# Performance work log

Hardware: AMD Instinct MI355X
Metric: run time of the kernel (lower is better)

The kernel has to match this reference:

```python
import jax, jax.numpy as jnp
import numpy as np

H = W = 96                      # image_size (scaled down from (240,240) for working-set control)
K = 16                          # faces_per_pixel
SIGMA = 1e-4
GAMMA = 1e-4
BLUR = float(np.log(1.0 / 1e-4 - 1.0) * SIGMA)   # blur_radius, compared against squared NDC dist (pytorch3d convention)
ZNEAR, ZFAR = 1.0, 100.0        # softmax_rgb_blend defaults
EPS = 1e-10


def _edge_d2(p, a, b):
    # squared point-to-segment distance; p:[B,P,F,2], a,b:[B,1,F,2]
    ab = b - a
    ap = p - a
    t = jnp.clip((ap * ab).sum(-1) / ((ab * ab).sum(-1) + 1e-12), 0.0, 1.0)
    d = ap - t[..., None] * ab
    return (d * d).sum(-1)


def _render(meshes_positions, meshes_rotations, meshes_scale, cam_pos, cam_rot, vertices, vert_colors, faces_packed):
    B, M, _ = meshes_positions.shape
    V = vertices.shape[1]
    # per-mesh scale -> rotate -> translate (forward of MeshesRenderer)
    scaled = meshes_scale[:, :, None, :] * vertices[None]                           # [B,M,V,3]
    world = jnp.einsum('bmij,bmvj->bmvi', meshes_rotations, scaled) + meshes_positions[:, :, None, :]
    world = world.reshape(B, M * V, 3)
    # pytorch3d camera: X_cam = X_world @ R + T
    cam = jnp.einsum('bvj,bji->bvi', world, cam_rot) + cam_pos[:, None, :]
    z = cam[..., 2]                                                                 # [B,N]
    xy = cam[..., :2] / z[..., None]                                                # perspective, focal=1 (NDC)

    tri = xy[:, faces_packed]                                                       # [B,F,3,2]
    tz = z[:, faces_packed]                                                         # [B,F,3]
    fcol = vert_colors.reshape(M * V, 3)[faces_packed]                              # [F,3,3]

    xs = (jnp.arange(W, dtype=xy.dtype) + 0.5) * 2.0 / W - 1.0
    ys = 1.0 - (jnp.arange(H, dtype=xy.dtype) + 0.5) * 2.0 / H
    gx, gy = jnp.meshgrid(xs, ys)
    pix = jnp.stack([gx.ravel(), gy.ravel()], -1)[None, :, None, :]                 # [1,P,1,2]

    v0 = tri[:, None, :, 0]; v1 = tri[:, None, :, 1]; v2 = tri[:, None, :, 2]       # [B,1,F,2]
    e1 = v1 - v0; e2 = v2 - v0
    d = pix - v0                                                                    # [B,P,F,2]
    den = e1[..., 0] * e2[..., 1] - e1[..., 1] * e2[..., 0] + 1e-12
    b1 = (d[..., 0] * e2[..., 1] - d[..., 1] * e2[..., 0]) / den                    # barycentrics [B,P,F]
    b2 = (e1[..., 0] * d[..., 1] - e1[..., 1] * d[..., 0]) / den
    b0 = 1.0 - b1 - b2
    zpix = b0 * tz[:, None, :, 0] + b1 * tz[:, None, :, 1] + b2 * tz[:, None, :, 2]
    inside = (b0 >= 0) & (b1 >= 0) & (b2 >= 0)
    d2 = jnp.minimum(jnp.minimum(_edge_d2(pix, v0, v1), _edge_d2(pix, v1, v2)), _edge_d2(pix, v2, v0))
    dists = jnp.where(inside, -d2, d2)                                              # signed squared dist
    valid = (zpix > 1e-2) & (dists <= BLUR)

    # faces_per_pixel = K nearest faces by depth (z-buffer)
    _, idx = jax.lax.top_k(jnp.where(valid, -zpix, -jnp.inf), K)                    # [B,P,K]
    take = lambda a: jnp.take_along_axis(a, idx, axis=-1)
    bk = jnp.stack([take(b0), take(b1), take(b2)], -1)                              # [B,P,K,3]
    zk, dk = take(zpix), take(dists)
    mk = take(valid.astype(zpix.dtype))
    # texture gather: barycentric blend of per-vertex colors (TexturesVertex.sample_textures)
    texel = jnp.einsum('bpkv,bpkvc->bpkc', bk, fcol[idx])                           # [B,P,K,3]

    # softmax_rgb_blend
    prob = jax.nn.sigmoid(-dk / SIGMA) * mk
    zinv = (ZFAR - zk) / (ZFAR - ZNEAR) * mk
    zmax = jnp.maximum(zinv.max(-1), EPS)
    wnum = prob * jnp.exp((zinv - zmax[..., None]) / GAMMA)
    delta = jnp.exp((EPS - zmax) / GAMMA)
    denom = wnum.sum(-1) + delta
    bg = jnp.ones(3, zpix.dtype)                                                    # default white background
    rgb = ((wnum[..., None] * texel).sum(-2) + delta[..., None] * bg) / denom[..., None]
    alpha = 1.0 - jnp.prod(1.0 - prob, -1)
    return jnp.concatenate([rgb, alpha[..., None]], -1).reshape(B, H, W, 4)


def setup_inputs() -> dict:
    key = jax.random.key(0)
    ks = jax.random.split(key, 8)
    B, M, V, Fm = 2, 2, 256, 256
    vertices = jax.random.normal(ks[0], (M, V, 3), jnp.float32) * 0.4
    faces = jax.random.randint(ks[1], (M, Fm, 3), 0, V)
    vert_colors = jax.random.uniform(ks[2], (M, V, 3), dtype=jnp.float32)
    meshes_positions = jax.random.normal(ks[3], (B, M, 3), jnp.float32) * 0.2
    # small z-axis rotations (proper rotation matrices)
    ang = jax.random.normal(ks[4], (B, M), jnp.float32) * 0.2
    c, s = jnp.cos(ang), jnp.sin(ang)
    z0 = jnp.zeros_like(c); o = jnp.ones_like(c)
    meshes_rotations = jnp.stack([c, -s, z0, s, c, z0, z0, z0, o], -1).reshape(B, M, 3, 3)
    meshes_scale = 1.0 + 0.1 * jax.random.normal(ks[5], (B, M, 3), jnp.float32)
    cam_rot = jnp.tile(jnp.eye(3, dtype=jnp.float32)[None], (B, 1, 1))
    cam_pos = jnp.tile(jnp.array([0.0, 0.0, 3.0], jnp.float32), (B, 1))
    return {
        'meshes_positions': meshes_positions, 'meshes_rotations': meshes_rotations,
        'meshes_scale': meshes_scale, 'cam_pos': cam_pos, 'cam_rot': cam_rot,
        'vertices': vertices, 'faces': faces, 'vert_colors': vert_colors,
    }


def reference(meshes_positions, meshes_rotations, meshes_scale, cam_pos, cam_rot, vertices, faces, vert_colors):
    M, V = vertices.shape[:2]
    faces_packed = (faces + (jnp.arange(M) * V)[:, None, None]).reshape(-1, 3)      # [F,3]
    return _render(meshes_positions, meshes_rotations, meshes_scale, cam_pos, cam_rot,
                   vertices, vert_colors, faces_packed)
```

## Files before the change

kernel.cpp:

```cpp
#include <hip/hip_runtime.h>

#pragma clang fp contract(off)

#define HH 96
#define WW 96
#define KK 16
#define MM 2
#define NF 512
#define NV 512
#define NPIX (HH*WW)
#define TDIM 12
#define TSZ 8
#define NTILE (TDIM*TDIM)
#define MAXC 8
#define BPT 8

#define SIGMA_F 1e-4f
#define GAMMA_F 1e-4f
#define BLUR_F  9.210240366975851e-4f
#define EPS_F   1e-10f
#define ZFAR_F  100.0f
#define ZNEAR_F 1.0f
#define RM      0.0304f

#define SENT 0xFFFFFFFFFFFFFFFFull

__device__ __forceinline__ float frcp(float x) { return __builtin_amdgcn_rcpf(x); }

__device__ __forceinline__ float edge_d2(float px, float py,
                                         float ax, float ay,
                                         float bx, float by) {
    float abx = bx - ax, aby = by - ay;
    float apx = px - ax, apy = py - ay;
    float t = (apx*abx + apy*aby) * frcp(abx*abx + aby*aby + 1e-12f);
    t = fminf(fmaxf(t, 0.0f), 1.0f);
    float dx = apx - t*abx, dy = apy - t*aby;
    return dx*dx + dy*dy;
}

struct Rast { float b0, b1, b2, zpix, dists; };

__device__ __forceinline__ Rast rasterize_s(float px, float py,
                                            float v0x, float v0y, float v1x, float v1y,
                                            float v2x, float v2y,
                                            float z0, float z1, float z2) {
    Rast r;
    float e1x=v1x-v0x, e1y=v1y-v0y, e2x=v2x-v0x, e2y=v2y-v0y;
    float dx=px-v0x, dy=py-v0y;
    float rden = frcp(e1x*e2y - e1y*e2x + 1e-12f);
    r.b1 = (dx*e2y - dy*e2x) * rden;
    r.b2 = (e1x*dy - e1y*dx) * rden;
    r.b0 = 1.0f - r.b1 - r.b2;
    r.zpix = r.b0*z0 + r.b1*z1 + r.b2*z2;
    bool inside = (r.b0 >= 0.0f) && (r.b1 >= 0.0f) && (r.b2 >= 0.0f);
    float d2 = edge_d2(px, py, v0x, v0y, v1x, v1y);
    d2 = fminf(d2, edge_d2(px, py, v1x, v1y, v2x, v2y));
    d2 = fminf(d2, edge_d2(px, py, v2x, v2y, v0x, v0y));
    r.dists = inside ? -d2 : d2;
    return r;
}

__device__ __forceinline__ unsigned long long packzf(float z, int f) {
    return (((unsigned long long)__float_as_uint(z)) << 32) | (unsigned int)f;
}

__device__ __forceinline__ unsigned long long shflx64(unsigned long long v, int m) {
    int lo = __shfl_xor((int)(unsigned)(v & 0xffffffffull), m, 64);
    int hi = __shfl_xor((int)(unsigned)(v >> 32), m, 64);
    return ((unsigned long long)(unsigned)hi << 32) | (unsigned)lo;
}

__global__ __launch_bounds__(512) void render_fused_kernel(
    const float* __restrict__ mpos,
    const float* __restrict__ mrot,
    const float* __restrict__ mscale,
    const float* __restrict__ cpos,
    const float* __restrict__ crot,
    const float* __restrict__ verts,
    const int*   __restrict__ faces,
    const float* __restrict__ vcol,
    float*       __restrict__ out)
{
    const int blocksPerB = NTILE * BPT;
    const int b    = blockIdx.x / blocksPerB;
    const int rem  = blockIdx.x % blocksPerB;
    const int tile = rem / BPT, q = rem % BPT;
    const int wv   = threadIdx.x >> 6;
    const int lane = threadIdx.x & 63;
    const int t    = threadIdx.x;

    __shared__ float svx[NV], svy[NV], svz[NV];
    __shared__ float scr_[NV], scg_[NV], scb_[NV];
    __shared__ float sbx0[NF], sby0[NF], sbx1[NF], sby1[NF];
    __shared__ int   si0[NF], si1[NF], si2[NF];
    __shared__ unsigned short slist[NF];

    float cr[9];
    #pragma unroll
    for (int i = 0; i < 9; ++i) cr[i] = crot[b*9 + i];
    const float cpx = cpos[b*3+0], cpy = cpos[b*3+1], cpz = cpos[b*3+2];

    {
        int g = t;
        int m = g >> 8;
        int sb = (b*MM + m)*3, rb = (b*MM + m)*9;
        float v0 = verts[g*3+0] * mscale[sb+0];
        float v1 = verts[g*3+1] * mscale[sb+1];
        float v2 = verts[g*3+2] * mscale[sb+2];
        float wx = mrot[rb+0]*v0 + mrot[rb+1]*v1 + mrot[rb+2]*v2 + mpos[sb+0];
        float wy = mrot[rb+3]*v0 + mrot[rb+4]*v1 + mrot[rb+5]*v2 + mpos[sb+1];
        float wz = mrot[rb+6]*v0 + mrot[rb+7]*v1 + mrot[rb+8]*v2 + mpos[sb+2];
        float cx = wx*cr[0] + wy*cr[3] + wz*cr[6] + cpx;
        float cy = wx*cr[1] + wy*cr[4] + wz*cr[7] + cpy;
        float cz = wx*cr[2] + wy*cr[5] + wz*cr[8] + cpz;
        svx[g] = cx / cz;  svy[g] = cy / cz;  svz[g] = cz;
        scr_[g] = vcol[g*3+0];
        scg_[g] = vcol[g*3+1];
        scb_[g] = vcol[g*3+2];
    }
    __syncthreads();

    {
        int f = t;
        int off = (f >> 8) << 8;
        int i0 = faces[f*3+0] + off;
        int i1 = faces[f*3+1] + off;
        int i2 = faces[f*3+2] + off;
        si0[f] = i0; si1[f] = i1; si2[f] = i2;
        float x0 = svx[i0], y0 = svy[i0];
        float x1 = svx[i1], y1 = svy[i1];
        float x2 = svx[i2], y2 = svy[i2];
        sbx0[f] = fminf(fminf(x0,x1),x2);
        sby0[f] = fminf(fminf(y0,y1),y2);
        sbx1[f] = fmaxf(fmaxf(x0,x1),x2);
        sby1[f] = fmaxf(fmaxf(y0,y1),y2);
    }
    __syncthreads();

    const int ty = tile / TDIM, tx = tile % TDIM;
    const float x_lo = -1.0f + tx * (2.0f / TDIM);
    const float x_hi = x_lo + 2.0f / TDIM;
    const float y_hi = 1.0f - ty * (2.0f / TDIM);
    const float y_lo = y_hi - 2.0f / TDIM;

    int L = 0;
    #pragma unroll
    for (int k = 0; k < 8; ++k) {
        int f = (k << 6) | lane;
        bool hit = (sbx0[f] - RM <= x_hi) && (sbx1[f] + RM >= x_lo) &&
                   (sby0[f] - RM <= y_hi) && (sby1[f] + RM >= y_lo);
        unsigned long long m = __ballot(hit);
        if (hit) {
            int rank = __popcll(m & ((1ull << lane) - 1ull));
            slist[L + rank] = (unsigned short)f;
        }
        L += __popcll(m);
    }

    const int pi = ty * TSZ + q, pj = tx * TSZ + wv;
    const float px = ((float)pj + 0.5f) * (2.0f / WW) - 1.0f;
    const float py = 1.0f - ((float)pi + 0.5f) * (2.0f / HH);

    unsigned long long pk[MAXC];
    int validm = 0;
    #pragma unroll
    for (int c = 0; c < MAXC; ++c) {
        pk[c] = SENT;
        if (c * 64 < L) {
            int idx = c * 64 + lane;
            int fc = (idx < L) ? (int)slist[idx] : -1;
            unsigned long long tt = SENT;
            if (fc >= 0) {
                int i0 = si0[fc], i1 = si1[fc], i2 = si2[fc];
                Rast r = rasterize_s(px, py, svx[i0], svy[i0], svx[i1], svy[i1],
                                     svx[i2], svy[i2], svz[i0], svz[i1], svz[i2]);
                if (r.zpix > 0.01f && r.dists <= BLUR_F) tt = packzf(r.zpix, fc);
            }
            pk[c] = tt;
            validm |= (tt != SENT ? 1 : 0) << c;
        }
    }

    const int c0 = __popc(validm);
    int cnt = c0;
    #pragma unroll
    for (int m = 1; m < 64; m <<= 1) cnt += __shfl_xor(cnt, m, 64);

    float nr = 0.0f, ng = 0.0f, nb = 0.0f, dn = 0.0f, ap = 1.0f;
    float zmaxv = EPS_F;

#define AGG(ff, zz) do { \
        int f_ = (ff); float z_ = (zz); \
        int i0_ = si0[f_], i1_ = si1[f_], i2_ = si2[f_]; \
        Rast r_ = rasterize_s(px, py, svx[i0_], svy[i0_], svx[i1_], svy[i1_], \
                              svx[i2_], svy[i2_], svz[i0_], svz[i1_], svz[i2_]); \
        float prob_ = frcp(1.0f + __expf(r_.dists / SIGMA_F)); \
        float zinv_ = (ZFAR_F - z_) / (ZFAR_F - ZNEAR_F); \
        float w_ = prob_ * __expf((zinv_ - zmaxv) / GAMMA_F); \
        nr += w_ * (r_.b0*scr_[i0_] + r_.b1*scr_[i1_] + r_.b2*scr_[i2_]); \
        ng += w_ * (r_.b0*scg_[i0_] + r_.b1*scg_[i1_] + r_.b2*scg_[i2_]); \
        nb += w_ * (r_.b0*scb_[i0_] + r_.b1*scb_[i1_] + r_.b2*scb_[i2_]); \
        dn += w_; \
        ap *= (1.0f - prob_); \
    } while (0)

    if (cnt <= KK) {
        unsigned long long lmin = pk[0];
        #pragma unroll
        for (int c = 1; c < MAXC; ++c) lmin = (pk[c] < lmin) ? pk[c] : lmin;
        #pragma unroll
        for (int m = 1; m < 64; m <<= 1) {
            unsigned long long o2 = shflx64(lmin, m);
            lmin = (o2 < lmin) ? o2 : lmin;
        }
        if (cnt > 0) {
            float zming = __uint_as_float((unsigned)(lmin >> 32));
            zmaxv = fmaxf((ZFAR_F - zming) / (ZFAR_F - ZNEAR_F), EPS_F);
        }
        #pragma unroll
        for (int c = 0; c < MAXC; ++c)
            if (validm & (1 << c)) {
                int f = (int)(pk[c] & 0xffffffffull);
                float z = __uint_as_float((unsigned)(pk[c] >> 32));
                AGG(f, z);
            }
    } else if (L <= 64) {
        unsigned long long v = pk[0];
        #pragma unroll
        for (int kk = 2; kk <= 64; kk <<= 1) {
            #pragma unroll
            for (int jj = kk >> 1; jj > 0; jj >>= 1) {
                unsigned long long o2 = shflx64(v, jj);
                bool kmin = ((lane & kk) == 0) == ((lane & jj) == 0);
                v = (kmin == (o2 < v)) ? o2 : v;
            }
        }
        unsigned z0b = (unsigned)__shfl((int)(unsigned)(v >> 32), 0, 64);
        zmaxv = fmaxf((ZFAR_F - __uint_as_float(z0b)) / (ZFAR_F - ZNEAR_F), EPS_F);
        if (lane < KK) {
            int f = (int)(v & 0xffffffffull);
            float z = __uint_as_float((unsigned)(v >> 32));
            AGG(f, z);
        }
    } else {
        int remm = validm, inclm = 0;
        float zming = 0.0f;
        for (int r = 0; r < KK; ++r) {
            unsigned long long lm = SENT;
            #pragma unroll
            for (int k = 0; k < MAXC; ++k)
                if (remm & (1 << k)) lm = (pk[k] < lm) ? pk[k] : lm;
            #pragma unroll
            for (int m = 1; m < 64; m <<= 1) {
                unsigned long long o2 = shflx64(lm, m);
                lm = (o2 < lm) ? o2 : lm;
            }
            if (r == 0) zming = __uint_as_float((unsigned)(lm >> 32));
            #pragma unroll
            for (int k = 0; k < MAXC; ++k)
                if ((remm & (1 << k)) && pk[k] == lm) { inclm |= 1 << k; remm &= ~(1 << k); }
        }
        zmaxv = fmaxf((ZFAR_F - zming) / (ZFAR_F - ZNEAR_F), EPS_F);
        #pragma unroll
        for (int k = 0; k < MAXC; ++k)
            if (inclm & (1 << k)) {
                int f = (int)(pk[k] & 0xffffffffull);
                float z = __uint_as_float((unsigned)(pk[k] >> 32));
                AGG(f, z);
            }
    }
#undef AGG

    #pragma unroll
    for (int m = 1; m < 64; m <<= 1) {
        nr += __shfl_xor(nr, m, 64);
        ng += __shfl_xor(ng, m, 64);
        nb += __shfl_xor(nb, m, 64);
        dn += __shfl_xor(dn, m, 64);
        ap *= __shfl_xor(ap, m, 64);
    }
    if (lane == 0) {
        float delta = __expf((EPS_F - zmaxv) / GAMMA_F);
        float dd = dn + delta;
        float4 o4;
        o4.x = (nr + delta) / dd;
        o4.y = (ng + delta) / dd;
        o4.z = (nb + delta) / dd;
        o4.w = 1.0f - ap;
        *reinterpret_cast<float4*>(&out[((size_t)b * NPIX + pi * WW + pj) * 4]) = o4;
    }
}

extern "C" void kernel_launch(void* const* d_in, const int* in_sizes, int n_in,
                              void* d_out, int out_size, void* d_ws, size_t ws_size,
                              hipStream_t stream) {
    const float* mpos   = (const float*)d_in[0];
    const float* mrot   = (const float*)d_in[1];
    const float* mscale = (const float*)d_in[2];
    const float* cpos   = (const float*)d_in[3];
    const float* crot   = (const float*)d_in[4];
    const float* verts  = (const float*)d_in[5];
    const int*   faces  = (const int*)d_in[6];
    const float* vcol   = (const float*)d_in[7];
    float*       out    = (float*)d_out;

    const int B = in_sizes[3] / 3;
    dim3 grid(B * NTILE * BPT), block(512);
    render_fused_kernel<<<grid, block, 0, stream>>>(
        mpos, mrot, mscale, cpos, crot, verts, faces, vcol, out);
}
```

Measured before the change: 45.15 us.

## Pack LDS vertex data, precompact face vertex indices, schedule tiles center-outward

```diff
diff --git a/kernel.cpp b/kernel.cpp
--- a/kernel.cpp
+++ b/kernel.cpp
@@ -60,14 +60,30 @@
     return r;
 }
 
-__device__ __forceinline__ unsigned long long packzf(float z, int f) {
-    return (((unsigned long long)__float_as_uint(z)) << 32) | (unsigned int)f;
+__device__ __forceinline__ unsigned long long packzf(float z, int id) {
+    return (((unsigned long long)__float_as_uint(z)) << 32) | (unsigned int)id;
 }
 
 __device__ __forceinline__ unsigned long long shflx64(unsigned long long v, int m) {
     int lo = __shfl_xor((int)(unsigned)(v & 0xffffffffull), m, 64);
     int hi = __shfl_xor((int)(unsigned)(v >> 32), m, 64);
     return ((unsigned long long)(unsigned)hi << 32) | (unsigned)lo;
+}
+
+__device__ __forceinline__ int ring_tile(int ord) {
+    int r = ((int)__builtin_sqrtf((float)ord)) >> 1;
+    while ((2*r+2)*(2*r+2) <= ord) ++r;
+    while (r > 0 && (2*r)*(2*r) > ord) --r;
+    int p = ord - 4*r*r;
+    int side = 2*r + 2;
+    int lo = TDIM/2 - 1 - r;
+    int hi = TDIM/2 + r;
+    int tx, ty;
+    if (p < side)              { ty = lo; tx = lo + p; }
+    else if (p < 2*side - 1)   { tx = hi; ty = lo + (p - side + 1); }
+    else if (p < 3*side - 2)   { ty = hi; tx = hi - (p - (2*side - 1) + 1); }
+    else                       { tx = lo; ty = hi - (p - (3*side - 2) + 1); }
+    return ty * TDIM + tx;
 }
 
 __global__ __launch_bounds__(512) void render_fused_kernel(
@@ -84,16 +100,18 @@
     const int blocksPerB = NTILE * BPT;
     const int b    = blockIdx.x / blocksPerB;
     const int rem  = blockIdx.x % blocksPerB;
-    const int tile = rem / BPT, q = rem % BPT;
+    const int tile = ring_tile(rem / BPT);
+    const int q    = rem % BPT;
     const int wv   = threadIdx.x >> 6;
     const int lane = threadIdx.x & 63;
     const int t    = threadIdx.x;
 
-    __shared__ float svx[NV], svy[NV], svz[NV];
-    __shared__ float scr_[NV], scg_[NV], scb_[NV];
-    __shared__ float sbx0[NF], sby0[NF], sbx1[NF], sby1[NF];
-    __shared__ int   si0[NF], si1[NF], si2[NF];
-    __shared__ unsigned short slist[NF];
+    __shared__ float2 svxy[NV];
+    __shared__ float  svz[NV];
+    __shared__ float4 scol[NV];
+    __shared__ float  sbx0[NF], sby0[NF], sbx1[NF], sby1[NF];
+    __shared__ int    si0[NF], si1[NF], si2[NF];
+    __shared__ int    cl0[NF], cl1[NF], cl2[NF];
 
     float cr[9];
     #pragma unroll
@@ -113,10 +131,9 @@
         float cx = wx*cr[0] + wy*cr[3] + wz*cr[6] + cpx;
         float cy = wx*cr[1] + wy*cr[4] + wz*cr[7] + cpy;
         float cz = wx*cr[2] + wy*cr[5] + wz*cr[8] + cpz;
-        svx[g] = cx / cz;  svy[g] = cy / cz;  svz[g] = cz;
-        scr_[g] = vcol[g*3+0];
-        scg_[g] = vcol[g*3+1];
-        scb_[g] = vcol[g*3+2];
+        svxy[g] = make_float2(cx / cz, cy / cz);
+        svz[g]  = cz;
+        scol[g] = make_float4(vcol[g*3+0], vcol[g*3+1], vcol[g*3+2], 0.0f);
     }
     __syncthreads();
 
@@ -127,13 +144,11 @@
         int i1 = faces[f*3+1] + off;
         int i2 = faces[f*3+2] + off;
         si0[f] = i0; si1[f] = i1; si2[f] = i2;
-        float x0 = svx[i0], y0 = svy[i0];
-        float x1 = svx[i1], y1 = svy[i1];
-        float x2 = svx[i2], y2 = svy[i2];
-        sbx0[f] = fminf(fminf(x0,x1),x2);
-        sby0[f] = fminf(fminf(y0,y1),y2);
-        sbx1[f] = fmaxf(fmaxf(x0,x1),x2);
-        sby1[f] = fmaxf(fmaxf(y0,y1),y2);
+        float2 p0 = svxy[i0], p1 = svxy[i1], p2 = svxy[i2];
+        sbx0[f] = fminf(fminf(p0.x,p1.x),p2.x);
+        sby0[f] = fminf(fminf(p0.y,p1.y),p2.y);
+        sbx1[f] = fmaxf(fmaxf(p0.x,p1.x),p2.x);
+        sby1[f] = fmaxf(fmaxf(p0.y,p1.y),p2.y);
     }
     __syncthreads();
 
@@ -143,16 +158,31 @@
     const float y_hi = 1.0f - ty * (2.0f / TDIM);
     const float y_lo = y_hi - 2.0f / TDIM;
 
-    int L = 0;
+    float bx0[8], by0[8], bx1[8], by1[8];
     #pragma unroll
     for (int k = 0; k < 8; ++k) {
         int f = (k << 6) | lane;
-        bool hit = (sbx0[f] - RM <= x_hi) && (sbx1[f] + RM >= x_lo) &&
-                   (sby0[f] - RM <= y_hi) && (sby1[f] + RM >= y_lo);
+        bx0[k] = sbx0[f]; by0[k] = sby0[f];
+        bx1[k] = sbx1[f]; by1[k] = sby1[f];
+    }
+    int hitm = 0;
+    #pragma unroll
+    for (int k = 0; k < 8; ++k) {
+        bool hit = (bx0[k] - RM <= x_hi) && (bx1[k] + RM >= x_lo) &&
+                   (by0[k] - RM <= y_hi) && (by1[k] + RM >= y_lo);
+        hitm |= (hit ? 1 : 0) << k;
+    }
+    int L = 0;
+    #pragma unroll
+    for (int k = 0; k < 8; ++k) {
+        bool hit = (hitm >> k) & 1;
         unsigned long long m = __ballot(hit);
         if (hit) {
-            int rank = __popcll(m & ((1ull << lane) - 1ull));
-            slist[L + rank] = (unsigned short)f;
+            int f = (k << 6) | lane;
+            int pos = L + __popcll(m & ((1ull << lane) - 1ull));
+            cl0[pos] = si0[f];
+            cl1[pos] = si1[f];
+            cl2[pos] = si2[f];
         }
         L += __popcll(m);
     }
@@ -168,13 +198,14 @@
         pk[c] = SENT;
         if (c * 64 < L) {
             int idx = c * 64 + lane;
-            int fc = (idx < L) ? (int)slist[idx] : -1;
             unsigned long long tt = SENT;
-            if (fc >= 0) {
-                int i0 = si0[fc], i1 = si1[fc], i2 = si2[fc];
-                Rast r = rasterize_s(px, py, svx[i0], svy[i0], svx[i1], svy[i1],
-                                     svx[i2], svy[i2], svz[i0], svz[i1], svz[i2]);
-                if (r.zpix > 0.01f && r.dists <= BLUR_F) tt = packzf(r.zpix, fc);
+            if (idx < L) {
+                int i0 = cl0[idx], i1 = cl1[idx], i2 = cl2[idx];
+                float2 p0 = svxy[i0], p1 = svxy[i1], p2 = svxy[i2];
+                float z0 = svz[i0], z1 = svz[i1], z2 = svz[i2];
+                Rast r = rasterize_s(px, py, p0.x, p0.y, p1.x, p1.y,
+                                     p2.x, p2.y, z0, z1, z2);
+                if (r.zpix > 0.01f && r.dists <= BLUR_F) tt = packzf(r.zpix, idx);
             }
             pk[c] = tt;
             validm |= (tt != SENT ? 1 : 0) << c;
@@ -189,17 +220,20 @@
     float nr = 0.0f, ng = 0.0f, nb = 0.0f, dn = 0.0f, ap = 1.0f;
     float zmaxv = EPS_F;
 
-#define AGG(ff, zz) do { \
-        int f_ = (ff); float z_ = (zz); \
-        int i0_ = si0[f_], i1_ = si1[f_], i2_ = si2[f_]; \
-        Rast r_ = rasterize_s(px, py, svx[i0_], svy[i0_], svx[i1_], svy[i1_], \
-                              svx[i2_], svy[i2_], svz[i0_], svz[i1_], svz[i2_]); \
+#define AGG(pp, zz) do { \
+        int p_ = (pp); float z_ = (zz); \
+        int i0_ = cl0[p_], i1_ = cl1[p_], i2_ = cl2[p_]; \
+        float2 q0_ = svxy[i0_], q1_ = svxy[i1_], q2_ = svxy[i2_]; \
+        float z0_ = svz[i0_], z1_ = svz[i1_], z2_ = svz[i2_]; \
+        Rast r_ = rasterize_s(px, py, q0_.x, q0_.y, q1_.x, q1_.y, \
+                              q2_.x, q2_.y, z0_, z1_, z2_); \
         float prob_ = frcp(1.0f + __expf(r_.dists / SIGMA_F)); \
         float zinv_ = (ZFAR_F - z_) / (ZFAR_F - ZNEAR_F); \
         float w_ = prob_ * __expf((zinv_ - zmaxv) / GAMMA_F); \
-        nr += w_ * (r_.b0*scr_[i0_] + r_.b1*scr_[i1_] + r_.b2*scr_[i2_]); \
-        ng += w_ * (r_.b0*scg_[i0_] + r_.b1*scg_[i1_] + r_.b2*scg_[i2_]); \
-        nb += w_ * (r_.b0*scb_[i0_] + r_.b1*scb_[i1_] + r_.b2*scb_[i2_]); \
+        float4 c0_ = scol[i0_], c1_ = scol[i1_], c2_ = scol[i2_]; \
+        nr += w_ * (r_.b0*c0_.x + r_.b1*c1_.x + r_.b2*c2_.x); \
+        ng += w_ * (r_.b0*c0_.y + r_.b1*c1_.y + r_.b2*c2_.y); \
+        nb += w_ * (r_.b0*c0_.z + r_.b1*c1_.z + r_.b2*c2_.z); \
         dn += w_; \
         ap *= (1.0f - prob_); \
     } while (0)
@@ -220,9 +254,9 @@
         #pragma unroll
         for (int c = 0; c < MAXC; ++c)
             if (validm & (1 << c)) {
-                int f = (int)(pk[c] & 0xffffffffull);
+                int id = (int)(pk[c] & 0xffffffffull);
                 float z = __uint_as_float((unsigned)(pk[c] >> 32));
-                AGG(f, z);
+                AGG(id, z);
             }
     } else if (L <= 64) {
         unsigned long long v = pk[0];
@@ -238,9 +272,9 @@
         unsigned z0b = (unsigned)__shfl((int)(unsigned)(v >> 32), 0, 64);
         zmaxv = fmaxf((ZFAR_F - __uint_as_float(z0b)) / (ZFAR_F - ZNEAR_F), EPS_F);
         if (lane < KK) {
-            int f = (int)(v & 0xffffffffull);
+            int id = (int)(v & 0xffffffffull);
             float z = __uint_as_float((unsigned)(v >> 32));
-            AGG(f, z);
+            AGG(id, z);
         }
     } else {
         int remm = validm, inclm = 0;
@@ -264,9 +298,9 @@
         #pragma unroll
         for (int k = 0; k < MAXC; ++k)
             if (inclm & (1 << k)) {
-                int f = (int)(pk[k] & 0xffffffffull);
+                int id = (int)(pk[k] & 0xffffffffull);
                 float z = __uint_as_float((unsigned)(pk[k] >> 32));
-                AGG(f, z);
+                AGG(id, z);
             }
     }
 #undef AGG
```

New measurement: 39.19 us, median of 2. -13.2%, faster.
